# Performance work log

Measured on AMD Instinct MI355X. Metric: run time of the kernel, lower is better.

## Reference

```python
import jax, jax.numpy as jnp
import numpy as np

N = 4096      # num_nodes
F = 256       # node_dim
K = 4         # num_heads
FP = 64       # out_dim per head
P_EDGE = 0.008  # edge probability (~33 avg degree)


def setup_inputs() -> dict:
    key = jax.random.key(0)
    k1, k2, k3, k4, k5 = jax.random.split(key, 5)
    x = jax.random.normal(k1, (N, F), dtype=jnp.float32)
    # binary adjacency mask with self loops so every row has a neighbor
    adj = (jax.random.uniform(k2, (N, N)) < P_EDGE).astype(jnp.float32)
    mask = jnp.maximum(adj, jnp.eye(N, dtype=jnp.float32))
    batch = jnp.zeros((N,), dtype=jnp.int32)  # unused (is_final_layer=False)
    # xavier-style init for W (node_dim -> K*FP) and attention vectors
    w_scale = np.sqrt(2.0 / (F + K * FP)).astype(np.float32)
    W = jax.random.normal(k3, (F, K * FP), dtype=jnp.float32) * w_scale
    b = jnp.zeros((K * FP,), dtype=jnp.float32)
    a_scale = np.sqrt(2.0 / (K * FP + 1)).astype(np.float32)
    a_left = jax.random.normal(k4, (1, K, FP), dtype=jnp.float32) * a_scale
    a_right = jax.random.normal(k5, (1, K, FP), dtype=jnp.float32) * a_scale
    return {"x": x, "mask": mask, "batch": batch, "W": W, "b": b,
            "a_left": a_left, "a_right": a_right}


def reference(x, mask, batch, W, b, a_left, a_right):
    # dropout prob = 0.0 (eval mode) -> identity
    x_proj = (x @ W + b).reshape(N, K, FP)                 # (N,K,F')
    score_src = (x_proj * a_left).sum(axis=-1)             # (N,K)
    score_tgt = (x_proj * a_right).sum(axis=-1)            # (N,K)
    score = score_src[:, None, :] + score_tgt[None, :, :]  # (N,N,K)
    score = jax.nn.leaky_relu(score, negative_slope=0.2)
    # non-standard global mean/std normalization (torch .std() is unbiased)
    score = (score - score.mean()) / score.std(ddof=1)
    score = jnp.exp(score)
    m = mask[:, :, None]                                   # (N,N,1)
    denom = (score * m).sum(axis=1, keepdims=True)         # (N,1,K)
    aij = (score / denom) * m                              # (N,N,K)
    attention = jnp.transpose(aij, (2, 0, 1))              # (K,N,N)
    h_prime = jnp.einsum('knm,mkf->nkf', attention, x_proj)  # (N,K,F')
    h_prime = jax.nn.elu(h_prime)
    # is_final_layer=False -> concat heads
    return h_prime.reshape(N, K * FP)
```

## Files before the change

kernel.cpp:

```cpp
#include <hip/hip_runtime.h>
#include <hip/hip_bf16.h>
#include <math.h>

#define NN 4096
#define FF 256
#define KH 4
#define FP 64
#define NCOL 256
#define MAXNBR 512
#define GEMM_BLKS 512
#define MOM_BLOCKS 512

__device__ __forceinline__ float bits2f(unsigned b) {
    union { unsigned u; float f; } c; c.u = b << 16; return c.f;
}
__device__ __forceinline__ int is_fp32(const void* mask) {
    return ((const unsigned*)mask)[0] == 0x3F800000u;
}

#define OFF_PART   0
#define OFF_XP     65536
#define OFF_SRC    4259840
#define OFF_TGT    4325376
#define OFF_NBR    4390912
#define OFF_CNT    8585216

__global__ __launch_bounds__(256) void k_gemm_scan(
        const void* __restrict__ xr, const void* __restrict__ mask,
        const void* __restrict__ Wr, const void* __restrict__ br,
        const void* __restrict__ alr, const void* __restrict__ arr,
        float* __restrict__ xp, float* __restrict__ srcb, float* __restrict__ tgtb,
        unsigned short* __restrict__ nbr_g, int* __restrict__ cnt_g) {
    const int fl = is_fp32(mask);
    const int tid = threadIdx.x;
    __shared__ union {
        float4 xs[8][64];
        struct { unsigned short snbr[MAXNBR]; int cnt; } sc;
    } sm;

    if (blockIdx.x >= GEMM_BLKS) {
        int n = blockIdx.x - GEMM_BLKS;
        if (tid == 0) sm.sc.cnt = 0;
        __syncthreads();
        if (fl) {
            const uint4* p = (const uint4*)((const float*)mask + (size_t)n * NN);
            for (int i = tid; i < NN / 4; i += 256) {
                uint4 v = p[i]; int base = i * 4;
                if (v.x) { int s = atomicAdd(&sm.sc.cnt, 1); if (s < MAXNBR) sm.sc.snbr[s] = base + 0; }
                if (v.y) { int s = atomicAdd(&sm.sc.cnt, 1); if (s < MAXNBR) sm.sc.snbr[s] = base + 1; }
                if (v.z) { int s = atomicAdd(&sm.sc.cnt, 1); if (s < MAXNBR) sm.sc.snbr[s] = base + 2; }
                if (v.w) { int s = atomicAdd(&sm.sc.cnt, 1); if (s < MAXNBR) sm.sc.snbr[s] = base + 3; }
            }
        } else {
            const uint4* p = (const uint4*)((const unsigned short*)mask + (size_t)n * NN);
            for (int i = tid; i < NN / 8; i += 256) {
                uint4 v = p[i]; int base = i * 8;
                if (v.x & 0xFFFFu) { int s = atomicAdd(&sm.sc.cnt, 1); if (s < MAXNBR) sm.sc.snbr[s] = base + 0; }
                if (v.x >> 16)     { int s = atomicAdd(&sm.sc.cnt, 1); if (s < MAXNBR) sm.sc.snbr[s] = base + 1; }
                if (v.y & 0xFFFFu) { int s = atomicAdd(&sm.sc.cnt, 1); if (s < MAXNBR) sm.sc.snbr[s] = base + 2; }
                if (v.y >> 16)     { int s = atomicAdd(&sm.sc.cnt, 1); if (s < MAXNBR) sm.sc.snbr[s] = base + 3; }
                if (v.z & 0xFFFFu) { int s = atomicAdd(&sm.sc.cnt, 1); if (s < MAXNBR) sm.sc.snbr[s] = base + 4; }
                if (v.z >> 16)     { int s = atomicAdd(&sm.sc.cnt, 1); if (s < MAXNBR) sm.sc.snbr[s] = base + 5; }
                if (v.w & 0xFFFFu) { int s = atomicAdd(&sm.sc.cnt, 1); if (s < MAXNBR) sm.sc.snbr[s] = base + 6; }
                if (v.w >> 16)     { int s = atomicAdd(&sm.sc.cnt, 1); if (s < MAXNBR) sm.sc.snbr[s] = base + 7; }
            }
        }
        __syncthreads();
        int c = sm.sc.cnt < MAXNBR ? sm.sc.cnt : MAXNBR;
        for (int j = tid; j < c; j += 256)
            nbr_g[(size_t)n * MAXNBR + j] = sm.sc.snbr[j];
        if (tid == 0) cnt_g[n] = c;
        return;
    }

    int n0 = blockIdx.x * 8;
    if (fl) {
        const float4* xq = (const float4*)xr;
        for (int t = tid; t < 512; t += 256) {
            int r = t >> 6, q = t & 63;
            sm.xs[r][q] = xq[(size_t)(n0 + r) * 64 + q];
        }
    } else {
        const ushort4* xq = (const ushort4*)xr;
        for (int t = tid; t < 512; t += 256) {
            int r = t >> 6, q = t & 63;
            ushort4 u = xq[(size_t)(n0 + r) * 64 + q];
            float4 v; v.x = bits2f(u.x); v.y = bits2f(u.y); v.z = bits2f(u.z); v.w = bits2f(u.w);
            sm.xs[r][q] = v;
        }
    }
    __syncthreads();
    int c = tid;
    float acc[8] = {};
    if (fl) {
        const float* WF = (const float*)Wr;
        for (int kk = 0; kk < 64; ++kk) {
            float w0 = WF[(4 * kk + 0) * NCOL + c];
            float w1 = WF[(4 * kk + 1) * NCOL + c];
            float w2 = WF[(4 * kk + 2) * NCOL + c];
            float w3 = WF[(4 * kk + 3) * NCOL + c];
            #pragma unroll
            for (int r = 0; r < 8; ++r) {
                float4 xv = sm.xs[r][kk];
                acc[r] += xv.x * w0 + xv.y * w1 + xv.z * w2 + xv.w * w3;
            }
        }
    } else {
        const unsigned short* WB = (const unsigned short*)Wr;
        for (int kk = 0; kk < 64; ++kk) {
            float w0 = bits2f(WB[(4 * kk + 0) * NCOL + c]);
            float w1 = bits2f(WB[(4 * kk + 1) * NCOL + c]);
            float w2 = bits2f(WB[(4 * kk + 2) * NCOL + c]);
            float w3 = bits2f(WB[(4 * kk + 3) * NCOL + c]);
            #pragma unroll
            for (int r = 0; r < 8; ++r) {
                float4 xv = sm.xs[r][kk];
                acc[r] += xv.x * w0 + xv.y * w1 + xv.z * w2 + xv.w * w3;
            }
        }
    }
    float bv, alv, arv;
    if (fl) {
        bv  = ((const float*)br)[c];
        alv = ((const float*)alr)[c];
        arv = ((const float*)arr)[c];
    } else {
        bv  = bits2f(((const unsigned short*)br)[c]);
        alv = bits2f(((const unsigned short*)alr)[c]);
        arv = bits2f(((const unsigned short*)arr)[c]);
    }
    int wave = tid >> 6;
    int lane = tid & 63;
    #pragma unroll
    for (int r = 0; r < 8; ++r) {
        float o = acc[r] + bv;
        xp[(size_t)(n0 + r) * NCOL + c] = o;
        float sr = o * alv, tr = o * arv;
        #pragma unroll
        for (int off = 32; off; off >>= 1) {
            sr += __shfl_down(sr, off, 64);
            tr += __shfl_down(tr, off, 64);
        }
        if (lane == 0) {
            srcb[(n0 + r) * KH + wave] = sr;
            tgtb[(n0 + r) * KH + wave] = tr;
        }
    }
}

__global__ __launch_bounds__(256) void k_moments(
        const float* __restrict__ srcb, const float* __restrict__ tgtb,
        double2* __restrict__ partials) {
    int id = blockIdx.x * 256 + threadIdx.x;
    int m = id & 4095;
    int nb = id >> 12;
    float4 tv = ((const float4*)tgtb)[m];
    float s1 = 0.f, s2 = 0.f;
    for (int n = nb; n < NN; n += 32) {
        float4 sv = ((const float4*)srcb)[n];
        float v0 = sv.x + tv.x; v0 = v0 > 0.f ? v0 : 0.2f * v0;
        float v1 = sv.y + tv.y; v1 = v1 > 0.f ? v1 : 0.2f * v1;
        float v2 = sv.z + tv.z; v2 = v2 > 0.f ? v2 : 0.2f * v2;
        float v3 = sv.w + tv.w; v3 = v3 > 0.f ? v3 : 0.2f * v3;
        s1 += v0 + v1 + v2 + v3;
        s2 += v0 * v0 + v1 * v1 + v2 * v2 + v3 * v3;
    }
    __shared__ double l1[256], l2[256];
    l1[threadIdx.x] = (double)s1;
    l2[threadIdx.x] = (double)s2;
    __syncthreads();
    for (int off = 128; off; off >>= 1) {
        if (threadIdx.x < off) {
            l1[threadIdx.x] += l1[threadIdx.x + off];
            l2[threadIdx.x] += l2[threadIdx.x + off];
        }
        __syncthreads();
    }
    if (threadIdx.x == 0) {
        double2 pr; pr.x = l1[0]; pr.y = l2[0];
        partials[blockIdx.x] = pr;
    }
}

__global__ __launch_bounds__(256) void k_aggregate(
        const unsigned short* __restrict__ nbr_g, const int* __restrict__ cnt_g,
        const double2* __restrict__ partials,
        const float* __restrict__ xp,
        const float* __restrict__ srcb, const float* __restrict__ tgtb,
        float* __restrict__ out) {
    const int tid = threadIdx.x;
    __shared__ union {
        struct { double l1[256], l2[256]; } red;
        struct {
            unsigned short snbr[MAXNBR];
            float pls[MAXNBR * KH];
            float invden[KH];
        } agg;
    } sm;
    __shared__ float mu_s, isg_s;

    {
        double a = 0.0, b2 = 0.0;
        #pragma unroll
        for (int i = 0; i < 2; ++i) {
            double2 pr = partials[tid + 256 * i];
            a += pr.x; b2 += pr.y;
        }
        sm.red.l1[tid] = a;
        sm.red.l2[tid] = b2;
        __syncthreads();
        for (int off = 128; off; off >>= 1) {
            if (tid < off) {
                sm.red.l1[tid] += sm.red.l1[tid + off];
                sm.red.l2[tid] += sm.red.l2[tid + off];
            }
            __syncthreads();
        }
        if (tid == 0) {
            double s = sm.red.l1[0], ss = sm.red.l2[0];
            const double tot = (double)NN * (double)NN * (double)KH;
            mu_s = (float)(s / tot);
            isg_s = (float)(1.0 / sqrt((ss - s * s / tot) / (tot - 1.0)));
        }
        __syncthreads();
    }
    float mu = mu_s, inv_sigma = isg_s;
    int n = blockIdx.x;
    int c = cnt_g[n];
    for (int j = tid; j < c; j += 256) sm.agg.snbr[j] = nbr_g[(size_t)n * MAXNBR + j];
    __syncthreads();

    for (int t = tid; t < c * KH; t += 256) {
        int j = t >> 2, k = t & 3;
        int m = sm.agg.snbr[j];
        float v = srcb[n * KH + k] + tgtb[m * KH + k];
        v = v > 0.f ? v : 0.2f * v;
        sm.agg.pls[j * KH + k] = expf((v - mu) * inv_sigma);
    }
    __syncthreads();
    if (tid < KH) {
        float d = 0.f;
        for (int j = 0; j < c; ++j) d += sm.agg.pls[j * KH + tid];
        sm.agg.invden[tid] = 1.0f / d;
    }
    __syncthreads();

    int col = tid;
    int k = col >> 6;
    float acc = 0.f;
    for (int j = 0; j < c; ++j) {
        acc += sm.agg.pls[j * KH + k] * xp[(size_t)sm.agg.snbr[j] * NCOL + col];
    }
    acc *= sm.agg.invden[k];
    float o = acc > 0.f ? acc : expm1f(acc);
    out[(size_t)n * NCOL + col] = o;
}

extern "C" void kernel_launch(void* const* d_in, const int* in_sizes, int n_in,
                              void* d_out, int out_size, void* d_ws, size_t ws_size,
                              hipStream_t stream) {
    const void* x    = d_in[0];
    const void* mask = d_in[1];
    const void* W    = d_in[3];
    const void* b    = d_in[4];
    const void* al   = d_in[5];
    const void* ar   = d_in[6];

    char* ws = (char*)d_ws;
    double2* part = (double2*)(ws + OFF_PART);
    float* xp   = (float*)(ws + OFF_XP);
    float* src  = (float*)(ws + OFF_SRC);
    float* tgt  = (float*)(ws + OFF_TGT);
    unsigned short* nbr = (unsigned short*)(ws + OFF_NBR);
    int* cntg = (int*)(ws + OFF_CNT);

    k_gemm_scan<<<GEMM_BLKS + NN, 256, 0, stream>>>(x, mask, W, b, al, ar,
                                                    xp, src, tgt, nbr, cntg);
    k_moments<<<MOM_BLOCKS, 256, 0, stream>>>(src, tgt, part);
    k_aggregate<<<NN, 256, 0, stream>>>(nbr, cntg, part, xp, src, tgt,
                                        (float*)d_out);
}
```

Before: 178.6 us.

## Widen moments grid and hoist mean/std fold into separate kernel

The moments kernel now uses 4096 blocks with a flat grid-stride loop over all N*N pairs instead of 512 blocks each looping over 128 source rows, giving more parallelism. The final reduction of the partials into mean and inverse std moves out of every aggregate block into a single one-block fold kernel, so the 4096 aggregate blocks no longer each redo that reduction. The cost is an extra kernel launch, a serial single-block step, and a global tgt load on every iteration.

```diff
diff --git a/kernel.cpp b/kernel.cpp
--- a/kernel.cpp
+++ b/kernel.cpp
@@ -9,7 +9,7 @@
 #define NCOL 256
 #define MAXNBR 512
 #define GEMM_BLKS 512
-#define MOM_BLOCKS 512
+#define MOM_BLOCKS 4096
 
 __device__ __forceinline__ float bits2f(unsigned b) {
     union { unsigned u; float f; } c; c.u = b << 16; return c.f;
@@ -19,11 +19,12 @@
 }
 
 #define OFF_PART   0
-#define OFF_XP     65536
-#define OFF_SRC    4259840
-#define OFF_TGT    4325376
-#define OFF_NBR    4390912
-#define OFF_CNT    8585216
+#define OFF_MUSIG  65536
+#define OFF_XP     131072
+#define OFF_SRC    4325376
+#define OFF_TGT    4390912
+#define OFF_NBR    4456448
+#define OFF_CNT    8650752
 
 __global__ __launch_bounds__(256) void k_gemm_scan(
         const void* __restrict__ xr, const void* __restrict__ mask,
@@ -151,13 +152,14 @@
 __global__ __launch_bounds__(256) void k_moments(
         const float* __restrict__ srcb, const float* __restrict__ tgtb,
         double2* __restrict__ partials) {
-    int id = blockIdx.x * 256 + threadIdx.x;
-    int m = id & 4095;
-    int nb = id >> 12;
-    float4 tv = ((const float4*)tgtb)[m];
+    const int total = NN * NN;
+    const int stride = MOM_BLOCKS * 256;
     float s1 = 0.f, s2 = 0.f;
-    for (int n = nb; n < NN; n += 32) {
+    #pragma unroll 4
+    for (int p = blockIdx.x * 256 + threadIdx.x; p < total; p += stride) {
+        int n = p >> 12, m = p & 4095;
         float4 sv = ((const float4*)srcb)[n];
+        float4 tv = ((const float4*)tgtb)[m];
         float v0 = sv.x + tv.x; v0 = v0 > 0.f ? v0 : 0.2f * v0;
         float v1 = sv.y + tv.y; v1 = v1 > 0.f ? v1 : 0.2f * v1;
         float v2 = sv.z + tv.z; v2 = v2 > 0.f ? v2 : 0.2f * v2;
@@ -182,66 +184,60 @@
     }
 }
 
+__global__ __launch_bounds__(256) void k_fold(
+        const double2* __restrict__ partials, float* __restrict__ musig) {
+    double a = 0.0, b2 = 0.0;
+    for (int i = threadIdx.x; i < MOM_BLOCKS; i += 256) {
+        double2 pr = partials[i];
+        a += pr.x; b2 += pr.y;
+    }
+    __shared__ double l1[256], l2[256];
+    l1[threadIdx.x] = a;
+    l2[threadIdx.x] = b2;
+    __syncthreads();
+    for (int off = 128; off; off >>= 1) {
+        if (threadIdx.x < off) {
+            l1[threadIdx.x] += l1[threadIdx.x + off];
+            l2[threadIdx.x] += l2[threadIdx.x + off];
+        }
+        __syncthreads();
+    }
+    if (threadIdx.x == 0) {
+        double s = l1[0], ss = l2[0];
+        const double tot = (double)NN * (double)NN * (double)KH;
+        musig[0] = (float)(s / tot);
+        musig[1] = (float)(1.0 / sqrt((ss - s * s / tot) / (tot - 1.0)));
+    }
+}
+
 __global__ __launch_bounds__(256) void k_aggregate(
         const unsigned short* __restrict__ nbr_g, const int* __restrict__ cnt_g,
-        const double2* __restrict__ partials,
+        const float* __restrict__ musig,
         const float* __restrict__ xp,
         const float* __restrict__ srcb, const float* __restrict__ tgtb,
         float* __restrict__ out) {
     const int tid = threadIdx.x;
-    __shared__ union {
-        struct { double l1[256], l2[256]; } red;
-        struct {
-            unsigned short snbr[MAXNBR];
-            float pls[MAXNBR * KH];
-            float invden[KH];
-        } agg;
-    } sm;
-    __shared__ float mu_s, isg_s;
-
-    {
-        double a = 0.0, b2 = 0.0;
-        #pragma unroll
-        for (int i = 0; i < 2; ++i) {
-            double2 pr = partials[tid + 256 * i];
-            a += pr.x; b2 += pr.y;
-        }
-        sm.red.l1[tid] = a;
-        sm.red.l2[tid] = b2;
-        __syncthreads();
-        for (int off = 128; off; off >>= 1) {
-            if (tid < off) {
-                sm.red.l1[tid] += sm.red.l1[tid + off];
-                sm.red.l2[tid] += sm.red.l2[tid + off];
-            }
-            __syncthreads();
-        }
-        if (tid == 0) {
-            double s = sm.red.l1[0], ss = sm.red.l2[0];
-            const double tot = (double)NN * (double)NN * (double)KH;
-            mu_s = (float)(s / tot);
-            isg_s = (float)(1.0 / sqrt((ss - s * s / tot) / (tot - 1.0)));
-        }
-        __syncthreads();
-    }
-    float mu = mu_s, inv_sigma = isg_s;
+    __shared__ unsigned short snbr[MAXNBR];
+    __shared__ float pls[MAXNBR * KH];
+    __shared__ float invden[KH];
+    float mu = musig[0], inv_sigma = musig[1];
     int n = blockIdx.x;
     int c = cnt_g[n];
-    for (int j = tid; j < c; j += 256) sm.agg.snbr[j] = nbr_g[(size_t)n * MAXNBR + j];
+    for (int j = tid; j < c; j += 256) snbr[j] = nbr_g[(size_t)n * MAXNBR + j];
     __syncthreads();
 
     for (int t = tid; t < c * KH; t += 256) {
         int j = t >> 2, k = t & 3;
-        int m = sm.agg.snbr[j];
+        int m = snbr[j];
         float v = srcb[n * KH + k] + tgtb[m * KH + k];
         v = v > 0.f ? v : 0.2f * v;
-        sm.agg.pls[j * KH + k] = expf((v - mu) * inv_sigma);
+        pls[j * KH + k] = expf((v - mu) * inv_sigma);
     }
     __syncthreads();
     if (tid < KH) {
         float d = 0.f;
-        for (int j = 0; j < c; ++j) d += sm.agg.pls[j * KH + tid];
-        sm.agg.invden[tid] = 1.0f / d;
+        for (int j = 0; j < c; ++j) d += pls[j * KH + tid];
+        invden[tid] = 1.0f / d;
     }
     __syncthreads();
 
@@ -249,9 +245,9 @@
     int k = col >> 6;
     float acc = 0.f;
     for (int j = 0; j < c; ++j) {
-        acc += sm.agg.pls[j * KH + k] * xp[(size_t)sm.agg.snbr[j] * NCOL + col];
-    }
-    acc *= sm.agg.invden[k];
+        acc += pls[j * KH + k] * xp[(size_t)snbr[j] * NCOL + col];
+    }
+    acc *= invden[k];
     float o = acc > 0.f ? acc : expm1f(acc);
     out[(size_t)n * NCOL + col] = o;
 }
@@ -268,6 +264,7 @@
 
     char* ws = (char*)d_ws;
     double2* part = (double2*)(ws + OFF_PART);
+    float* musig = (float*)(ws + OFF_MUSIG);
     float* xp   = (float*)(ws + OFF_XP);
     float* src  = (float*)(ws + OFF_SRC);
     float* tgt  = (float*)(ws + OFF_TGT);
@@ -277,6 +274,7 @@
     k_gemm_scan<<<GEMM_BLKS + NN, 256, 0, stream>>>(x, mask, W, b, al, ar,
                                                     xp, src, tgt, nbr, cntg);
     k_moments<<<MOM_BLOCKS, 256, 0, stream>>>(src, tgt, part);
-    k_aggregate<<<NN, 256, 0, stream>>>(nbr, cntg, part, xp, src, tgt,
+    k_fold<<<1, 256, 0, stream>>>(part, musig);
+    k_aggregate<<<NN, 256, 0, stream>>>(nbr, cntg, musig, xp, src, tgt,
                                         (float*)d_out);
 }
```

New measurement: 158.5 us. 11.3% less time.
